# Kernel tuning notes

Measured on AMD Instinct MI355X. Metric: run time of the kernel, lower is better.

## Reference

```python
import jax, jax.numpy as jnp
import numpy as np

NQ, NS, QN, SN = 10000, 500, 4, 10   # num_question, num_skill, q/s neighbor sizes
B, S, D = 32, 200, 128               # batch, seq_len, emb_dim
HOPS = 3


def setup_inputs() -> dict:
    key = jax.random.key(0)
    ks = iter(jax.random.split(key, 40))

    def nrm(shape, scale=0.05):
        return jax.random.normal(next(ks), shape, dtype=jnp.float32) * scale

    return {
        "question": jax.random.randint(next(ks), (B, S), 0, NQ),
        "response": jax.random.randint(next(ks), (B, S), 0, 2),
        "mask": jnp.ones((B, S), dtype=jnp.int32),
        "q_neighbors": jax.random.randint(next(ks), (NQ, QN), 0, NS),  # question -> skill ids
        "s_neighbors": jax.random.randint(next(ks), (NS, SN), 0, NQ),  # skill -> question ids
        "qs_skills": jax.random.randint(next(ks), (NQ, 4), 0, NS),     # related skills per question
        "emb_q": nrm((NQ, D), 1.0),
        "emb_s": nrm((NS, D), 1.0),
        "emb_r": nrm((2, D), 1.0),
        "W_ih": nrm((2 * D, 4 * D)), "b_ih": nrm((4 * D,)), "b_hh": nrm((4 * D,)),
        "ft_W": nrm((D, D)), "ft_b": nrm((D,)),
        "agg_W": nrm((HOPS, D, D)), "agg_b": nrm((HOPS, D)),
        "last_W": nrm((D, D)), "last_b": nrm((D,)),
        "q_W": nrm((D, D)), "q_b": nrm((D,)),
        "k_W": nrm((D, D)), "k_b": nrm((D,)),
        "w_W": nrm((2 * D,)), "w_b": nrm(()),
    }


def reference(question, response, mask, q_neighbors, s_neighbors, qs_skills,
              emb_q, emb_s, emb_r, W_ih, b_ih, b_hh, ft_W, ft_b,
              agg_W, agg_b, last_W, last_b, q_W, q_b, k_W, k_b, w_W, w_b):
    # ---- multi-hop GNN aggregation for every (b, t) question (mask == 1 everywhere) ----
    q_flat = question.reshape(-1)              # [B*S]
    lvl1 = q_neighbors[q_flat]                 # [N, QN]            skill ids
    lvl2 = s_neighbors[lvl1]                   # [N, QN, SN]        question ids
    lvl3 = q_neighbors[lvl2]                   # [N, QN, SN, QN]    skill ids
    embs = [emb_q[q_flat], emb_s[lvl1], emb_q[lvl2], emb_s[lvl3]]
    for i in range(HOPS):
        embs = [jnp.tanh((embs[j] + embs[j + 1].mean(axis=-2)) @ agg_W[j] + agg_b[j])
                for j in range(HOPS - i)]
    agg_emb = jnp.tanh(embs[0] @ last_W + last_b).reshape(B, S, D)

    # ---- per-step input + zero-state LSTMCell (source calls lstm_cell without hx) ----
    q_trans = jax.nn.relu(agg_emb @ ft_W + ft_b)
    x = jnp.concatenate([q_trans, emb_r[response]], axis=-1)   # [B, S, 2D]
    gates = x @ W_ih + b_ih + b_hh                             # h_prev = 0, c_prev = 0
    i_g, f_g, g_g, o_g = jnp.split(gates, 4, axis=-1)
    c = jax.nn.sigmoid(i_g) * jnp.tanh(g_g)
    h = jax.nn.sigmoid(o_g) * jnp.tanh(c)                      # [B, S, D]
    states = h[:, :S - 1]                                      # state written at step t

    # ---- soft-recap attention prediction for q_next = question[:, t+1] ----
    q_next = question[:, 1:]                                   # [B, T], T = S-1
    qs = jnp.concatenate([emb_q[q_next][:, :, None, :], emb_s[qs_skills[q_next]]], axis=2)  # [B,T,5,D]

    inner = jnp.einsum('bnd,btmd->btnm', states, qs)           # state/qs inner products
    a_state = (states @ q_W + q_b) @ w_W[:D]                   # [B, N]  MLP_query on states
    a_qs = (qs @ k_W + k_b) @ w_W[D:]                          # [B, T, 5] MLP_key on qs
    logits = a_state[:, None, :, None] + a_qs[:, :, None, :] + w_b  # [B, T, N, 5]

    t_idx = jnp.arange(S - 1)
    valid = t_idx[None, :] <= t_idx[:, None]                   # [T, N]: states 0..t visible at t
    logits = jnp.where(valid[None, :, :, None], logits, -jnp.inf)
    alpha = jax.nn.softmax(logits.reshape(B, S - 1, -1), axis=-1).reshape(logits.shape)
    pred = jnp.sum(alpha * jax.nn.sigmoid(inner), axis=(2, 3))  # [B, T]

    return jnp.zeros((B, S), jnp.float32).at[:, 1:].set(pred)
```

## Files before the change

### kernel.cpp

```cpp
#include <hip/hip_runtime.h>

typedef unsigned short u16;
typedef unsigned int   u32;

#define NQd 10000
#define NSd 500
#define Bd  32
#define Sd  200
#define Td  199
#define Dd  128
#define NR  6368
#define PB  208

typedef __attribute__((ext_vector_type(8))) short bf16x8;
typedef __attribute__((ext_vector_type(4))) float f32x4;

__device__ __forceinline__ float sigf(float x) {
  return __builtin_amdgcn_rcpf(1.f + __expf(-x));
}
__device__ __forceinline__ float tanh_f(float x) {
  float ax = fminf(fabsf(x), 15.f);
  float e = __expf(2.f * ax);
  float r = 1.f - 2.f * __builtin_amdgcn_rcpf(e + 1.f);
  return copysignf(r, x);
}
__device__ __forceinline__ float bf2f(u16 u) { return __uint_as_float(((u32)u) << 16); }
__device__ __forceinline__ u16 f2bf(float f) {
  u32 b = __float_as_uint(f);
  b += 0x7FFFu + ((b >> 16) & 1u);
  return (u16)(b >> 16);
}
__device__ __forceinline__ void unp2(u32 u, float &a, float &b) {
  a = __uint_as_float(u << 16);
  b = __uint_as_float(u & 0xffff0000u);
}
__device__ __forceinline__ void unpack16(uint4 a0, uint4 a1, float* f) {
  unp2(a0.x, f[0], f[1]);  unp2(a0.y, f[2], f[3]);
  unp2(a0.z, f[4], f[5]);  unp2(a0.w, f[6], f[7]);
  unp2(a1.x, f[8], f[9]);  unp2(a1.y, f[10], f[11]);
  unp2(a1.z, f[12], f[13]); unp2(a1.w, f[14], f[15]);
}

struct Args {
  const int *question, *response, *q_nb, *s_nb, *qs_sk;
  const float *emb_q, *emb_s, *emb_r;
  const float *W_ih, *b_ih, *b_hh, *ft_W, *ft_b, *agg_W, *agg_b, *last_W, *last_b;
  const float *q_W, *q_b, *k_W, *k_b, *w_W;
  u16 *tabA, *tabB, *tabC, *tabs1, *tabs2, *states, *embq_bf, *embs_bf, *wts, *wiht;
  float *a_state, *qw, *kw, *scal, *er_part, *ev, *invZ, *pred_acc, *pm;
  int *qid_map, *resp_map;
};

#define SMEM_U16 21760

__device__ __forceinline__ void mfma_accum(const u16* Al, const u16* Wl,
                                           int l15, int quad, int cw, f32x4 acc[2][2])
{
#pragma unroll
  for (int kc = 0; kc < 4; ++kc) {
    const int ko = kc * 32 + quad * 8;
    bf16x8 af[2], bfv[2];
    af[0]  = *(const bf16x8*)&Al[l15 * 136 + ko];
    af[1]  = *(const bf16x8*)&Al[(16 + l15) * 136 + ko];
    bfv[0] = *(const bf16x8*)&Wl[(cw + l15) * 136 + ko];
    bfv[1] = *(const bf16x8*)&Wl[(cw + 16 + l15) * 136 + ko];
#pragma unroll
    for (int mt = 0; mt < 2; ++mt)
#pragma unroll
      for (int nt = 0; nt < 2; ++nt)
        acc[mt][nt] = __builtin_amdgcn_mfma_f32_16x16x32_bf16(af[mt], bfv[nt], acc[mt][nt], 0, 0, 0);
  }
}

__device__ __forceinline__ void zero_acc(f32x4 acc[2][2]) {
#pragma unroll
  for (int x = 0; x < 2; ++x)
#pragma unroll
    for (int y = 0; y < 2; ++y) acc[x][y] = (f32x4){0.f, 0.f, 0.f, 0.f};
}

__device__ __forceinline__ void stage_A(const u16* Atab, const u16* Btab,
                                        const int* nbr, int K, int tile0, int rows,
                                        int tid, u16* Al)
{
  int r = tid & 31, k0 = (tid >> 5) * 16;
  int row = tile0 + r; if (row >= rows) row = rows - 1;
  const u16* ap = Atab + (long)row * 128 + k0;
  if (K == 0) {
    *(uint4*)&Al[r * 136 + k0]     = *(const uint4*)ap;
    *(uint4*)&Al[r * 136 + k0 + 8] = *(const uint4*)(ap + 8);
  } else {
    float f[16];
    unpack16(*(const uint4*)ap, *(const uint4*)(ap + 8), f);
    float s[16];
#pragma unroll
    for (int q = 0; q < 16; ++q) s[q] = 0.f;
    for (int l = 0; l < K; ++l) {
      int id = nbr[(long)row * K + l];
      const u16* np = Btab + (long)id * 128 + k0;
      float g[16];
      unpack16(*(const uint4*)np, *(const uint4*)(np + 8), g);
#pragma unroll
      for (int q = 0; q < 16; ++q) s[q] += g[q];
    }
    float inv = 1.f / (float)K;
#pragma unroll
    for (int q = 0; q < 16; ++q) f[q] += s[q] * inv;
    u32 p[8];
#pragma unroll
    for (int q = 0; q < 8; ++q)
      p[q] = (u32)f2bf(f[2 * q]) | ((u32)f2bf(f[2 * q + 1]) << 16);
    *(uint4*)&Al[r * 136 + k0]     = make_uint4(p[0], p[1], p[2], p[3]);
    *(uint4*)&Al[r * 136 + k0 + 8] = make_uint4(p[4], p[5], p[6], p[7]);
  }
}

__device__ __forceinline__ void stage_W(const u16* Wt, int tid, u16* Wl)
{
  for (int i = tid; i < 2048; i += 256) {
    int col = i >> 4, seg = i & 15;
    *(uint4*)&Wl[col * 136 + seg * 8] = *(const uint4*)&Wt[(long)col * 128 + seg * 8];
  }
}

__device__ __forceinline__ void epi_tanh_global(const f32x4 acc[2][2], const float* cbias,
                                                u16* out, int rows, int tile0,
                                                int l15, int quad, int cw)
{
#pragma unroll
  for (int nt = 0; nt < 2; ++nt) {
    int col = cw + nt * 16 + l15;
    float cb = cbias[col];
#pragma unroll
    for (int mt = 0; mt < 2; ++mt) {
      int rbase = tile0 + mt * 16 + quad * 4;
#pragma unroll
      for (int i = 0; i < 4; ++i) {
        int row = rbase + i;
        if (row >= rows) continue;
        out[(long)row * 128 + col] = f2bf(tanh_f(acc[mt][nt][i] + cb));
      }
    }
  }
}

__device__ __forceinline__ void gemm_tile(
    const u16* __restrict__ Atab, const u16* __restrict__ Btab,
    const int* __restrict__ nbr, int K,
    const u16* __restrict__ Wt, const float* __restrict__ cbias,
    u16* __restrict__ out, int rows, int tile0, int tid, u16* smem)
{
  u16* Wl = smem;
  u16* Al = smem + 17408;
  stage_W(Wt, tid, Wl);
  stage_A(Atab, Btab, nbr, K, tile0, rows, tid, Al);
  __syncthreads();
  const int lane = tid & 63, wv = tid >> 6;
  const int l15 = lane & 15, quad = lane >> 4, cw = wv * 32;
  f32x4 acc[2][2];
  zero_acc(acc);
  mfma_accum(Al, Wl, l15, quad, cw, acc);
  epi_tanh_global(acc, cbias, out, rows, tile0, l15, quad, cw);
}

__global__ __launch_bounds__(256) void prep_all(Args a)
{
  const int T = gridDim.x * 256;
  for (int i = blockIdx.x * 256 + threadIdx.x; i < 491106; i += T) {
    if (i < 320000) {
      float4 v = *(const float4*)&a.emb_q[(long)i * 4];
      ((uint2*)a.embq_bf)[i] = make_uint2(
          (u32)f2bf(v.x) | ((u32)f2bf(v.y) << 16),
          (u32)f2bf(v.z) | ((u32)f2bf(v.w) << 16));
    } else if (i < 336000) {
      int c = i - 320000;
      float4 v = *(const float4*)&a.emb_s[(long)c * 4];
      ((uint2*)a.embs_bf)[c] = make_uint2(
          (u32)f2bf(v.x) | ((u32)f2bf(v.y) << 16),
          (u32)f2bf(v.z) | ((u32)f2bf(v.w) << 16));
    } else if (i < 417920) {
      int e = i - 336000;
      int seg = e >> 14, r = e & 16383;
      int col = r >> 7, k = r & 127;
      const float* src = (seg < 3) ? (a.agg_W + seg * 16384)
                                   : (seg == 3 ? a.last_W : a.ft_W);
      a.wts[e] = f2bf(src[k * 128 + col]);
    } else if (i < 483456) {
      int e = i - 417920;
      int col = e >> 7, k = e & 127;
      a.wiht[e] = f2bf(a.W_ih[k * 512 + col]);
    } else if (i < 489824) {
      int j = i - 483456;
      int b = j / Td, s = j - b * Td;
      a.qid_map[j]  = a.question[b * Sd + s];
      a.resp_map[j] = a.response[b * Sd + s];
    } else {
      int s = i - 489824;
      if (s < 128) {
        float acc = 0;
        for (int e = 0; e < 128; ++e) acc += a.q_W[s * 128 + e] * a.w_W[e];
        a.qw[s] = acc;
      } else if (s < 256) {
        int d = s - 128; float acc = 0;
        for (int e = 0; e < 128; ++e) acc += a.k_W[d * 128 + e] * a.w_W[128 + e];
        a.kw[d] = acc;
      } else if (s == 256) {
        float acc = 0;
        for (int e = 0; e < 128; ++e) acc += a.q_b[e] * a.w_W[e];
        a.scal[0] = acc;
      } else if (s == 257) {
        float acc = 0;
        for (int e = 0; e < 128; ++e) acc += a.k_b[e] * a.w_W[128 + e];
        a.scal[1] = acc;
      } else {
        int e2 = s - 258, rr = e2 >> 9, col = e2 & 511;
        float acc = a.b_ih[col] + a.b_hh[col];
        for (int d = 0; d < 128; ++d) acc += a.emb_r[rr * Dd + d] * a.W_ih[(128 + d) * 512 + col];
        a.er_part[rr * 512 + col] = acc;
      }
    }
  }
}

__global__ __launch_bounds__(256) void level1m(Args a)
{
  __shared__ __align__(16) u16 smem[SMEM_U16];
  const int i = blockIdx.x, tid = threadIdx.x;
  if (i >= 313) {
    gemm_tile(a.embs_bf, a.embq_bf, a.s_nb, 10, a.wts + 16384,
              a.agg_b + 128, a.tabs1, NSd, (i - 313) * 32, tid, smem);
    return;
  }
  u16* Wl = smem;
  u16* Al = smem + 17408;
  const int tile0 = i * 32;
  const int lane = tid & 63, wv = tid >> 6;
  const int l15 = lane & 15, quad = lane >> 4, cw = wv * 32;
  f32x4 acc[2][2];
  stage_W(a.wts + 2 * 16384, tid, Wl);
  stage_A(a.embq_bf, a.embs_bf, a.q_nb, 4, tile0, NQd, tid, Al);
  __syncthreads();
  zero_acc(acc);
  mfma_accum(Al, Wl, l15, quad, cw, acc);
  epi_tanh_global(acc, a.agg_b + 256, a.tabA, NQd, tile0, l15, quad, cw);
  __syncthreads();
  stage_W(a.wts, tid, Wl);
  __syncthreads();
  zero_acc(acc);
  mfma_accum(Al, Wl, l15, quad, cw, acc);
  epi_tanh_global(acc, a.agg_b, a.tabB, NQd, tile0, l15, quad, cw);
}

__global__ __launch_bounds__(256) void level2(Args a)
{
  __shared__ __align__(16) u16 smem[SMEM_U16];
  const int i = blockIdx.x, tid = threadIdx.x;
  if (i < 16)
    gemm_tile(a.tabs1, a.tabA, a.s_nb, 10, a.wts + 16384,
              a.agg_b + 128, a.tabs2, NSd, i * 32, tid, smem);
  else
    gemm_tile(a.tabB, a.tabs1, a.q_nb, 4, a.wts,
              a.agg_b, a.tabC, NQd, (i - 16) * 32, tid, smem);
}

__global__ __launch_bounds__(256) void chain3(Args a)
{
  __shared__ __align__(16) u16 smem[SMEM_U16];
  u16* Wl = smem;
  u16* Al = smem + 17408;
  const int tid = threadIdx.x;
  const int tile0 = blockIdx.x * 32;
  const int lane = tid & 63, wv = tid >> 6;
  const int l15 = lane & 15, quad = lane >> 4, cw = wv * 32;
  f32x4 acc[2][2];

  stage_W(a.wts, tid, Wl);
  stage_A(a.tabC, a.tabs2, a.q_nb, 4, tile0, NQd, tid, Al);
  __syncthreads();
  zero_acc(acc);
  mfma_accum(Al, Wl, l15, quad, cw, acc);
  __syncthreads();
#pragma unroll
  for (int nt = 0; nt < 2; ++nt) {
    int col = cw + nt * 16 + l15;
    float cb = a.agg_b[col];
#pragma unroll
    for (int mt = 0; mt < 2; ++mt)
#pragma unroll
      for (int i = 0; i < 4; ++i) {
        int rL = mt * 16 + quad * 4 + i;
        Al[rL * 136 + col] = f2bf(tanh_f(acc[mt][nt][i] + cb));
      }
  }
  stage_W(a.wts + 3 * 16384, tid, Wl);
  __syncthreads();

  zero_acc(acc);
  mfma_accum(Al, Wl, l15, quad, cw, acc);
  __syncthreads();
#pragma unroll
  for (int nt = 0; nt < 2; ++nt) {
    int col = cw + nt * 16 + l15;
    float cb = a.last_b[col];
#pragma unroll
    for (int mt = 0; mt < 2; ++mt)
#pragma unroll
      for (int i = 0; i < 4; ++i) {
        int rL = mt * 16 + quad * 4 + i;
        Al[rL * 136 + col] = f2bf(tanh_f(acc[mt][nt][i] + cb));
      }
  }
  stage_W(a.wts + 4 * 16384, tid, Wl);
  __syncthreads();

  zero_acc(acc);
  mfma_accum(Al, Wl, l15, quad, cw, acc);
#pragma unroll
  for (int nt = 0; nt < 2; ++nt) {
    int col = cw + nt * 16 + l15;
    float cb = a.ft_b[col];
#pragma unroll
    for (int mt = 0; mt < 2; ++mt) {
      int rbase = tile0 + mt * 16 + quad * 4;
#pragma unroll
      for (int i = 0; i < 4; ++i) {
        int row = rbase + i;
        if (row >= NQd) continue;
        a.tabA[(long)row * 128 + col] = f2bf(fmaxf(acc[mt][nt][i] + cb, 0.f));
      }
    }
  }
}

__global__ __launch_bounds__(256) void gates_k(Args a)
{
  __shared__ __align__(16) u16 smem[SMEM_U16];
  u16* Wl = smem;
  u16* Al = smem + 17408;
  const int tid = threadIdx.x;
  const int tile0 = blockIdx.x * 32;
  {
    int r = tid & 31, k0 = (tid >> 5) * 16;
    int row = tile0 + r;
    int arow = a.qid_map[row];
    const u16* ap = a.tabA + (long)arow * 128 + k0;
    *(uint4*)&Al[r * 136 + k0]     = *(const uint4*)ap;
    *(uint4*)&Al[r * 136 + k0 + 8] = *(const uint4*)(ap + 8);
  }
  const int lane = tid & 63, wv = tid >> 6;
  const int l15 = lane & 15, quad = lane >> 4, cw = wv * 32;
  f32x4 acc[3][2][2];
  const int goff[3] = {0, 256, 384};
#pragma unroll
  for (int p = 0; p < 3; ++p) {
    __syncthreads();
    stage_W(a.wiht + (long)goff[p] * 128, tid, Wl);
    __syncthreads();
    zero_acc(acc[p]);
    mfma_accum(Al, Wl, l15, quad, cw, acc[p]);
  }
  __syncthreads();
  float* hb = (float*)Wl;
#pragma unroll
  for (int nt = 0; nt < 2; ++nt) {
    int colL = cw + nt * 16 + l15;
#pragma unroll
    for (int mt = 0; mt < 2; ++mt) {
#pragma unroll
      for (int i = 0; i < 4; ++i) {
        int rL = mt * 16 + quad * 4 + i;
        int row = tile0 + rL;
        const float* rb = a.er_part + (long)a.resp_map[row] * 512;
        float iv = acc[0][mt][nt][i] + rb[colL];
        float gv = acc[1][mt][nt][i] + rb[256 + colL];
        float ov = acc[2][mt][nt][i] + rb[384 + colL];
        float c = sigf(iv) * tanh_f(gv);
        float h = sigf(ov) * tanh_f(c);
        a.states[(long)row * 128 + colL] = f2bf(h);
        hb[rL * 132 + colL] = h;
      }
    }
  }
  __syncthreads();
#pragma unroll
  for (int rr = 0; rr < 8; ++rr) {
    int rL = wv * 8 + rr;
    float p = hb[rL * 132 + lane] * a.qw[lane] + hb[rL * 132 + 64 + lane] * a.qw[64 + lane];
#pragma unroll
    for (int off = 32; off > 0; off >>= 1) p += __shfl_xor(p, off);
    if (lane == 0) a.a_state[tile0 + rL] = p + a.scal[0];
  }
}

__global__ __launch_bounds__(256) void bprep(Args a)
{
  __shared__ float red[256];
  __shared__ float evl[256];
  __shared__ float kwl[128];
  const int b = blockIdx.x, tid = threadIdx.x;
  if (tid < 128) kwl[tid] = a.kw[tid];
  float v = (tid < Td) ? a.a_state[b * Td + tid] : -1e30f;
  red[tid] = v; __syncthreads();
  for (int s = 128; s > 0; s >>= 1) { if (tid < s) red[tid] = fmaxf(red[tid], red[tid + s]); __syncthreads(); }
  float gmax = red[0];
  float e = (tid < Td) ? __expf(v - gmax) : 0.f;
  evl[tid] = e;
  if (tid < Td) { a.ev[b * PB + tid] = e; a.pred_acc[b * PB + tid] = 0.f; }
  __syncthreads();
  if (tid < Td) {
    float Z = 0.f;
    for (int n = 0; n <= tid; ++n) Z += evl[n];
    a.invZ[b * PB + tid] = 1.f / Z;
    int qn = a.question[b * Sd + tid + 1];
    float am[5];
#pragma unroll
    for (int m = 0; m < 5; ++m) {
      const u16* src = (m == 0) ? a.embq_bf + (long)qn * 128
                                : a.embs_bf + (long)a.qs_sk[qn * 4 + (m - 1)] * 128;
      float s = 0.f;
      for (int k = 0; k < 128; k += 8) {
        uint4 u = *(const uint4*)&src[k];
        float f[8];
        unp2(u.x, f[0], f[1]); unp2(u.y, f[2], f[3]);
        unp2(u.z, f[4], f[5]); unp2(u.w, f[6], f[7]);
#pragma unroll
        for (int q = 0; q < 8; ++q) s = fmaf(f[q], kwl[k + q], s);
      }
      am[m] = s + a.scal[1];
    }
    float mx = am[0];
#pragma unroll
    for (int m = 1; m < 5; ++m) mx = fmaxf(mx, am[m]);
    float ex[5], z = 0.f;
#pragma unroll
    for (int m = 0; m < 5; ++m) { ex[m] = __expf(am[m] - mx); z += ex[m]; }
    float iz = 1.f / z;
#pragma unroll
    for (int m = 0; m < 5; ++m) a.pm[((long)b * PB + tid) * 5 + m] = ex[m] * iz;
  }
}

__global__ __launch_bounds__(256) void gk_pred(Args a)
{
  const int n0 = blockIdx.x * 32;
  const int c0 = blockIdx.y * 128;
  const int b  = blockIdx.z;
  int c_hi = c0 + 127; if (c_hi > 994) c_hi = 994;
  const int tmax = c_hi / 5, tmin = c0 / 5;
  if (n0 > tmax) return;

  __shared__ __align__(16) u16 smem[SMEM_U16];
  __shared__ float predl[32];
  u16* Ql = smem;
  u16* Sl = smem + 17408;
  const int tid = threadIdx.x;
  if (tid < 32) predl[tid] = 0.f;
  {
    int r = tid & 31, k0 = (tid >> 5) * 16;
    int n = n0 + r; if (n > 198) n = 198;
    const u16* sp = a.states + ((long)b * Td + n) * 128 + k0;
    *(uint4*)&Sl[r * 136 + k0]     = *(const uint4*)sp;
    *(uint4*)&Sl[r * 136 + k0 + 8] = *(const uint4*)(sp + 8);
  }
  {
    int j = tid >> 1, k0 = (tid & 1) * 64;
    int col = c0 + j;
    uint4* dst = (uint4*)&Ql[j * 136 + k0];
    if (col < 995) {
      int t = col / 5, m = col - t * 5;
      int qn = a.question[b * Sd + t + 1];
      const u16* src = (m == 0) ? a.embq_bf + (long)qn * 128
                                : a.embs_bf + (long)a.qs_sk[qn * 4 + (m - 1)] * 128;
      src += k0;
#pragma unroll
      for (int q = 0; q < 8; ++q) dst[q] = ((const uint4*)src)[q];
    } else {
      uint4 z = make_uint4(0, 0, 0, 0);
#pragma unroll
      for (int q = 0; q < 8; ++q) dst[q] = z;
    }
  }
  __syncthreads();
  const int lane = tid & 63, wv = tid >> 6;
  const int l15 = lane & 15, quad = lane >> 4, cw = wv * 32;
  f32x4 acc[2][2];
  zero_acc(acc);
  mfma_accum(Sl, Ql, l15, quad, cw, acc);

#pragma unroll
  for (int nt = 0; nt < 2; ++nt) {
    int col = c0 + cw + nt * 16 + l15;
    if (col >= 995) continue;
    int t = col / 5, m = col - t * 5;
    float pmv = a.pm[((long)b * PB + t) * 5 + m];
    float part = 0.f;
#pragma unroll
    for (int mt = 0; mt < 2; ++mt) {
      int nb = n0 + mt * 16 + quad * 4;
      if (nb > t) continue;
      float4 ev4 = *(const float4*)&a.ev[b * PB + nb];
      float evv[4] = {ev4.x, ev4.y, ev4.z, ev4.w};
#pragma unroll
      for (int i = 0; i < 4; ++i) {
        int n = nb + i;
        if (n > t || n > 198) continue;
        part += evv[i] * sigf(acc[mt][nt][i]);
      }
    }
    part *= pmv;
    if (part != 0.f) atomicAdd(&predl[t - tmin], part);
  }
  __syncthreads();
  const int tcnt = tmax - tmin + 1;
  if (tid < tcnt) {
    float pv = predl[tid];
    if (pv != 0.f) atomicAdd(&a.pred_acc[b * PB + tmin + tid], pv);
  }
}

__global__ __launch_bounds__(256) void finalize(Args a, float* __restrict__ out)
{
  int i = blockIdx.x * 256 + threadIdx.x;
  if (i >= Bd * Sd) return;
  int b = i / Sd, s = i - b * Sd;
  out[i] = (s == 0) ? 0.f : a.pred_acc[b * PB + s - 1] * a.invZ[b * PB + s - 1];
}

extern "C" void kernel_launch(void* const* d_in, const int* in_sizes, int n_in,
                              void* d_out, int out_size, void* d_ws, size_t ws_size,
                              hipStream_t stream)
{
  Args a;
  a.question = (const int*)d_in[0];
  a.response = (const int*)d_in[1];
  a.q_nb     = (const int*)d_in[3];
  a.s_nb     = (const int*)d_in[4];
  a.qs_sk    = (const int*)d_in[5];
  a.emb_q    = (const float*)d_in[6];
  a.emb_s    = (const float*)d_in[7];
  a.emb_r    = (const float*)d_in[8];
  a.W_ih     = (const float*)d_in[9];
  a.b_ih     = (const float*)d_in[10];
  a.b_hh     = (const float*)d_in[11];
  a.ft_W     = (const float*)d_in[12];
  a.ft_b     = (const float*)d_in[13];
  a.agg_W    = (const float*)d_in[14];
  a.agg_b    = (const float*)d_in[15];
  a.last_W   = (const float*)d_in[16];
  a.last_b   = (const float*)d_in[17];
  a.q_W      = (const float*)d_in[18];
  a.q_b      = (const float*)d_in[19];
  a.k_W      = (const float*)d_in[20];
  a.k_b      = (const float*)d_in[21];
  a.w_W      = (const float*)d_in[22];

  u16* wsu = (u16*)d_ws;
  const long NT = 1280000, ST = 64000, RT = (long)NR * Dd;
  a.tabA  = wsu;
  a.tabB  = a.tabA + NT;
  a.tabC  = a.tabB + NT;
  a.tabs1 = a.tabC + NT;
  a.tabs2 = a.tabs1 + ST;
  a.states  = a.tabs2 + ST;
  a.embq_bf = a.states + RT;
  a.embs_bf = a.embq_bf + NT;
  a.wts     = a.embs_bf + ST;
  a.wiht    = a.wts + 5 * 16384;
  float* fp = (float*)(a.wiht + 65536);
  a.a_state = fp;
  a.qw      = fp + 6368;
  a.kw      = fp + 6496;
  a.scal    = fp + 6624;
  a.er_part = fp + 6640;
  a.ev       = fp + 7664;
  a.invZ     = a.ev + 32 * PB;
  a.pred_acc = a.invZ + 32 * PB;
  a.pm       = a.pred_acc + 32 * PB;
  a.qid_map  = (int*)(a.pm + 32 * PB * 5);
  a.resp_map = a.qid_map + NR;

  float* out = (float*)d_out;

  prep_all<<<640, 256, 0, stream>>>(a);
  level1m<<<329, 256, 0, stream>>>(a);
  level2<<<329, 256, 0, stream>>>(a);
  chain3<<<313, 256, 0, stream>>>(a);
  gates_k<<<199, 256, 0, stream>>>(a);
  bprep<<<Bd, 256, 0, stream>>>(a);
  gk_pred<<<dim3(7, 8, Bd), 256, 0, stream>>>(a);
  finalize<<<25, 256, 0, stream>>>(a, out);
}
```

Before: 196.7 us.

## Shrink GNN GEMM tiles to 16 rows and fuse level2 into chain kernel

The GEMM tiles in the GNN kernels shrink from 32x128 with 256 threads to 16x128 with 128 threads, doubling the block count so more compute units are busy. The tabC computation from level2 moves into the chain kernel, which keeps the intermediate in shared memory and reuses the staged neighbor ids. This removes one launch and a global round trip, leaving only a small skill-level kernel (g1k) separate. The serial prefix sum in bprep becomes a parallel Hillis-Steele scan. In exchange, each block now reloads the 128x128 weight tile for only 16 rows, which halves weight reuse per load.

After: 213.4 us. 8.5% more time.

```diff
diff --git a/kernel.cpp b/kernel.cpp
--- a/kernel.cpp
+++ b/kernel.cpp
@@ -51,39 +51,22 @@
   int *qid_map, *resp_map;
 };
 
-#define SMEM_U16 21760
-
-__device__ __forceinline__ void mfma_accum(const u16* Al, const u16* Wl,
-                                           int l15, int quad, int cw, f32x4 acc[2][2])
-{
-#pragma unroll
-  for (int kc = 0; kc < 4; ++kc) {
-    const int ko = kc * 32 + quad * 8;
-    bf16x8 af[2], bfv[2];
-    af[0]  = *(const bf16x8*)&Al[l15 * 136 + ko];
-    af[1]  = *(const bf16x8*)&Al[(16 + l15) * 136 + ko];
-    bfv[0] = *(const bf16x8*)&Wl[(cw + l15) * 136 + ko];
-    bfv[1] = *(const bf16x8*)&Wl[(cw + 16 + l15) * 136 + ko];
-#pragma unroll
-    for (int mt = 0; mt < 2; ++mt)
-#pragma unroll
-      for (int nt = 0; nt < 2; ++nt)
-        acc[mt][nt] = __builtin_amdgcn_mfma_f32_16x16x32_bf16(af[mt], bfv[nt], acc[mt][nt], 0, 0, 0);
-  }
-}
-
-__device__ __forceinline__ void zero_acc(f32x4 acc[2][2]) {
-#pragma unroll
-  for (int x = 0; x < 2; ++x)
-#pragma unroll
-    for (int y = 0; y < 2; ++y) acc[x][y] = (f32x4){0.f, 0.f, 0.f, 0.f};
-}
-
-__device__ __forceinline__ void stage_A(const u16* Atab, const u16* Btab,
-                                        const int* nbr, int K, int tile0, int rows,
-                                        int tid, u16* Al)
-{
-  int r = tid & 31, k0 = (tid >> 5) * 16;
+#define SM16_U16 (128 * 136 + 16 * 136)
+
+__device__ __forceinline__ void stageW128(const u16* Wt, int tid, u16* Wl)
+{
+  for (int i = tid; i < 2048; i += 128) {
+    int col = i >> 4, seg = i & 15;
+    *(uint4*)&Wl[col * 136 + seg * 8] = *(const uint4*)&Wt[(long)col * 128 + seg * 8];
+  }
+}
+
+template <int K>
+__device__ __forceinline__ void stageA16(const u16* Atab, const u16* Btab,
+                                         const int* nbr, int tile0, int rows,
+                                         int tid, u16* Al, int* ids)
+{
+  int r = tid & 15, k0 = (tid >> 4) * 16;
   int row = tile0 + r; if (row >= rows) row = rows - 1;
   const u16* ap = Atab + (long)row * 128 + k0;
   if (K == 0) {
@@ -95,15 +78,17 @@
     float s[16];
 #pragma unroll
     for (int q = 0; q < 16; ++q) s[q] = 0.f;
+#pragma unroll
+    for (int l = 0; l < K; ++l) ids[l] = nbr[(long)row * K + l];
+#pragma unroll
     for (int l = 0; l < K; ++l) {
-      int id = nbr[(long)row * K + l];
-      const u16* np = Btab + (long)id * 128 + k0;
+      const u16* np = Btab + (long)ids[l] * 128 + k0;
       float g[16];
       unpack16(*(const uint4*)np, *(const uint4*)(np + 8), g);
 #pragma unroll
       for (int q = 0; q < 16; ++q) s[q] += g[q];
     }
-    float inv = 1.f / (float)K;
+    const float inv = 1.f / (float)K;
 #pragma unroll
     for (int q = 0; q < 16; ++q) f[q] += s[q] * inv;
     u32 p[8];
@@ -115,52 +100,80 @@
   }
 }
 
-__device__ __forceinline__ void stage_W(const u16* Wt, int tid, u16* Wl)
-{
-  for (int i = tid; i < 2048; i += 256) {
-    int col = i >> 4, seg = i & 15;
-    *(uint4*)&Wl[col * 136 + seg * 8] = *(const uint4*)&Wt[(long)col * 128 + seg * 8];
-  }
-}
-
-__device__ __forceinline__ void epi_tanh_global(const f32x4 acc[2][2], const float* cbias,
-                                                u16* out, int rows, int tile0,
-                                                int l15, int quad, int cw)
-{
-#pragma unroll
-  for (int nt = 0; nt < 2; ++nt) {
-    int col = cw + nt * 16 + l15;
-    float cb = cbias[col];
-#pragma unroll
-    for (int mt = 0; mt < 2; ++mt) {
-      int rbase = tile0 + mt * 16 + quad * 4;
-#pragma unroll
-      for (int i = 0; i < 4; ++i) {
-        int row = rbase + i;
-        if (row >= rows) continue;
-        out[(long)row * 128 + col] = f2bf(tanh_f(acc[mt][nt][i] + cb));
-      }
-    }
-  }
-}
-
-__device__ __forceinline__ void gemm_tile(
-    const u16* __restrict__ Atab, const u16* __restrict__ Btab,
-    const int* __restrict__ nbr, int K,
-    const u16* __restrict__ Wt, const float* __restrict__ cbias,
-    u16* __restrict__ out, int rows, int tile0, int tid, u16* smem)
-{
-  u16* Wl = smem;
-  u16* Al = smem + 17408;
-  stage_W(Wt, tid, Wl);
-  stage_A(Atab, Btab, nbr, K, tile0, rows, tid, Al);
-  __syncthreads();
-  const int lane = tid & 63, wv = tid >> 6;
-  const int l15 = lane & 15, quad = lane >> 4, cw = wv * 32;
-  f32x4 acc[2][2];
-  zero_acc(acc);
-  mfma_accum(Al, Wl, l15, quad, cw, acc);
-  epi_tanh_global(acc, cbias, out, rows, tile0, l15, quad, cw);
+__device__ __forceinline__ void updateA16(const u16* Btab, const int* ids, int tid, u16* Al)
+{
+  int r = tid & 15, k0 = (tid >> 4) * 16;
+  float f[16];
+  unpack16(*(const uint4*)&Al[r * 136 + k0], *(const uint4*)&Al[r * 136 + k0 + 8], f);
+  float s[16];
+#pragma unroll
+  for (int q = 0; q < 16; ++q) s[q] = 0.f;
+#pragma unroll
+  for (int l = 0; l < 4; ++l) {
+    const u16* np = Btab + (long)ids[l] * 128 + k0;
+    float g[16];
+    unpack16(*(const uint4*)np, *(const uint4*)(np + 8), g);
+#pragma unroll
+    for (int q = 0; q < 16; ++q) s[q] += g[q];
+  }
+#pragma unroll
+  for (int q = 0; q < 16; ++q) f[q] += s[q] * 0.25f;
+  u32 p[8];
+#pragma unroll
+  for (int q = 0; q < 8; ++q)
+    p[q] = (u32)f2bf(f[2 * q]) | ((u32)f2bf(f[2 * q + 1]) << 16);
+  *(uint4*)&Al[r * 136 + k0]     = make_uint4(p[0], p[1], p[2], p[3]);
+  *(uint4*)&Al[r * 136 + k0 + 8] = make_uint4(p[4], p[5], p[6], p[7]);
+}
+
+__device__ __forceinline__ void zero4(f32x4 acc[4]) {
+#pragma unroll
+  for (int nt = 0; nt < 4; ++nt) acc[nt] = (f32x4){0.f, 0.f, 0.f, 0.f};
+}
+
+__device__ __forceinline__ void mfma16(const u16* Al, const u16* Wl,
+                                       int l15, int quad, int cw4, f32x4 acc[4])
+{
+#pragma unroll
+  for (int kc = 0; kc < 4; ++kc) {
+    const int ko = kc * 32 + quad * 8;
+    bf16x8 af = *(const bf16x8*)&Al[l15 * 136 + ko];
+#pragma unroll
+    for (int nt = 0; nt < 4; ++nt)
+      acc[nt] = __builtin_amdgcn_mfma_f32_16x16x32_bf16(
+          af, *(const bf16x8*)&Wl[(cw4 + nt * 16 + l15) * 136 + ko], acc[nt], 0, 0, 0);
+  }
+}
+
+__device__ __forceinline__ void epi_tanh_G16(const f32x4 acc[4], const float* cb,
+                                             u16* out, int rows, int tile0,
+                                             int l15, int quad, int cw4)
+{
+#pragma unroll
+  for (int nt = 0; nt < 4; ++nt) {
+    int col = cw4 + nt * 16 + l15;
+    float c = cb[col];
+#pragma unroll
+    for (int i = 0; i < 4; ++i) {
+      int row = tile0 + quad * 4 + i;
+      if (row < rows) out[(long)row * 128 + col] = f2bf(tanh_f(acc[nt][i] + c));
+    }
+  }
+}
+
+__device__ __forceinline__ void epi_tanh_L16(const f32x4 acc[4], const float* cb,
+                                             u16* Al, int l15, int quad, int cw4)
+{
+#pragma unroll
+  for (int nt = 0; nt < 4; ++nt) {
+    int col = cw4 + nt * 16 + l15;
+    float c = cb[col];
+#pragma unroll
+    for (int i = 0; i < 4; ++i) {
+      int rL = quad * 4 + i;
+      Al[rL * 136 + col] = f2bf(tanh_f(acc[nt][i] + c));
+    }
+  }
 }
 
 __global__ __launch_bounds__(256) void prep_all(Args a)
@@ -222,125 +235,117 @@
   }
 }
 
-__global__ __launch_bounds__(256) void level1m(Args a)
-{
-  __shared__ __align__(16) u16 smem[SMEM_U16];
+__global__ __launch_bounds__(128) void level1m(Args a)
+{
+  __shared__ __align__(16) u16 smem[SM16_U16];
+  u16* Wl = smem;
+  u16* Al = smem + 128 * 136;
   const int i = blockIdx.x, tid = threadIdx.x;
-  if (i >= 313) {
-    gemm_tile(a.embs_bf, a.embq_bf, a.s_nb, 10, a.wts + 16384,
-              a.agg_b + 128, a.tabs1, NSd, (i - 313) * 32, tid, smem);
+  const int lane = tid & 63, wv = tid >> 6;
+  const int l15 = lane & 15, quad = lane >> 4, cw4 = wv * 64;
+  f32x4 acc[4];
+  int ids[10];
+  if (i >= 625) {
+    const int tile0 = (i - 625) * 16;
+    stageW128(a.wts + 16384, tid, Wl);
+    stageA16<10>(a.embs_bf, a.embq_bf, a.s_nb, tile0, NSd, tid, Al, ids);
+    __syncthreads();
+    zero4(acc);
+    mfma16(Al, Wl, l15, quad, cw4, acc);
+    epi_tanh_G16(acc, a.agg_b + 128, a.tabs1, NSd, tile0, l15, quad, cw4);
     return;
   }
+  const int tile0 = i * 16;
+  stageW128(a.wts + 2 * 16384, tid, Wl);
+  stageA16<4>(a.embq_bf, a.embs_bf, a.q_nb, tile0, NQd, tid, Al, ids);
+  __syncthreads();
+  zero4(acc);
+  mfma16(Al, Wl, l15, quad, cw4, acc);
+  epi_tanh_G16(acc, a.agg_b + 256, a.tabA, NQd, tile0, l15, quad, cw4);
+  __syncthreads();
+  stageW128(a.wts, tid, Wl);
+  __syncthreads();
+  zero4(acc);
+  mfma16(Al, Wl, l15, quad, cw4, acc);
+  epi_tanh_G16(acc, a.agg_b, a.tabB, NQd, tile0, l15, quad, cw4);
+}
+
+__global__ __launch_bounds__(128) void g1k(Args a)
+{
+  __shared__ __align__(16) u16 smem[SM16_U16];
   u16* Wl = smem;
-  u16* Al = smem + 17408;
-  const int tile0 = i * 32;
+  u16* Al = smem + 128 * 136;
+  const int tid = threadIdx.x;
+  const int tile0 = blockIdx.x * 16;
   const int lane = tid & 63, wv = tid >> 6;
-  const int l15 = lane & 15, quad = lane >> 4, cw = wv * 32;
-  f32x4 acc[2][2];
-  stage_W(a.wts + 2 * 16384, tid, Wl);
-  stage_A(a.embq_bf, a.embs_bf, a.q_nb, 4, tile0, NQd, tid, Al);
-  __syncthreads();
-  zero_acc(acc);
-  mfma_accum(Al, Wl, l15, quad, cw, acc);
-  epi_tanh_global(acc, a.agg_b + 256, a.tabA, NQd, tile0, l15, quad, cw);
-  __syncthreads();
-  stage_W(a.wts, tid, Wl);
-  __syncthreads();
-  zero_acc(acc);
-  mfma_accum(Al, Wl, l15, quad, cw, acc);
-  epi_tanh_global(acc, a.agg_b, a.tabB, NQd, tile0, l15, quad, cw);
-}
-
-__global__ __launch_bounds__(256) void level2(Args a)
-{
-  __shared__ __align__(16) u16 smem[SMEM_U16];
-  const int i = blockIdx.x, tid = threadIdx.x;
-  if (i < 16)
-    gemm_tile(a.tabs1, a.tabA, a.s_nb, 10, a.wts + 16384,
-              a.agg_b + 128, a.tabs2, NSd, i * 32, tid, smem);
-  else
-    gemm_tile(a.tabB, a.tabs1, a.q_nb, 4, a.wts,
-              a.agg_b, a.tabC, NQd, (i - 16) * 32, tid, smem);
-}
-
-__global__ __launch_bounds__(256) void chain3(Args a)
-{
-  __shared__ __align__(16) u16 smem[SMEM_U16];
+  const int l15 = lane & 15, quad = lane >> 4, cw4 = wv * 64;
+  f32x4 acc[4];
+  int ids[10];
+  stageW128(a.wts + 16384, tid, Wl);
+  stageA16<10>(a.tabs1, a.tabA, a.s_nb, tile0, NSd, tid, Al, ids);
+  __syncthreads();
+  zero4(acc);
+  mfma16(Al, Wl, l15, quad, cw4, acc);
+  epi_tanh_G16(acc, a.agg_b + 128, a.tabs2, NSd, tile0, l15, quad, cw4);
+}
+
+__global__ __launch_bounds__(128) void chain4(Args a)
+{
+  __shared__ __align__(16) u16 smem[SM16_U16];
   u16* Wl = smem;
-  u16* Al = smem + 17408;
+  u16* Al = smem + 128 * 136;
   const int tid = threadIdx.x;
-  const int tile0 = blockIdx.x * 32;
+  const int tile0 = blockIdx.x * 16;
   const int lane = tid & 63, wv = tid >> 6;
-  const int l15 = lane & 15, quad = lane >> 4, cw = wv * 32;
-  f32x4 acc[2][2];
-
-  stage_W(a.wts, tid, Wl);
-  stage_A(a.tabC, a.tabs2, a.q_nb, 4, tile0, NQd, tid, Al);
-  __syncthreads();
-  zero_acc(acc);
-  mfma_accum(Al, Wl, l15, quad, cw, acc);
-  __syncthreads();
-#pragma unroll
-  for (int nt = 0; nt < 2; ++nt) {
-    int col = cw + nt * 16 + l15;
-    float cb = a.agg_b[col];
-#pragma unroll
-    for (int mt = 0; mt < 2; ++mt)
-#pragma unroll
-      for (int i = 0; i < 4; ++i) {
-        int rL = mt * 16 + quad * 4 + i;
-        Al[rL * 136 + col] = f2bf(tanh_f(acc[mt][nt][i] + cb));
-      }
-  }
-  stage_W(a.wts + 3 * 16384, tid, Wl);
-  __syncthreads();
-
-  zero_acc(acc);
-  mfma_accum(Al, Wl, l15, quad, cw, acc);
-  __syncthreads();
-#pragma unroll
-  for (int nt = 0; nt < 2; ++nt) {
-    int col = cw + nt * 16 + l15;
-    float cb = a.last_b[col];
-#pragma unroll
-    for (int mt = 0; mt < 2; ++mt)
-#pragma unroll
-      for (int i = 0; i < 4; ++i) {
-        int rL = mt * 16 + quad * 4 + i;
-        Al[rL * 136 + col] = f2bf(tanh_f(acc[mt][nt][i] + cb));
-      }
-  }
-  stage_W(a.wts + 4 * 16384, tid, Wl);
-  __syncthreads();
-
-  zero_acc(acc);
-  mfma_accum(Al, Wl, l15, quad, cw, acc);
-#pragma unroll
-  for (int nt = 0; nt < 2; ++nt) {
-    int col = cw + nt * 16 + l15;
+  const int l15 = lane & 15, quad = lane >> 4, cw4 = wv * 64;
+  f32x4 acc[4];
+  int ids[4];
+
+  stageW128(a.wts, tid, Wl);
+  stageA16<4>(a.tabB, a.tabs1, a.q_nb, tile0, NQd, tid, Al, ids);
+  __syncthreads();
+  zero4(acc);
+  mfma16(Al, Wl, l15, quad, cw4, acc);
+  __syncthreads();
+  epi_tanh_L16(acc, a.agg_b, Al, l15, quad, cw4);
+  __syncthreads();
+  updateA16(a.tabs2, ids, tid, Al);
+  __syncthreads();
+  zero4(acc);
+  mfma16(Al, Wl, l15, quad, cw4, acc);
+  __syncthreads();
+  epi_tanh_L16(acc, a.agg_b, Al, l15, quad, cw4);
+  stageW128(a.wts + 3 * 16384, tid, Wl);
+  __syncthreads();
+  zero4(acc);
+  mfma16(Al, Wl, l15, quad, cw4, acc);
+  __syncthreads();
+  epi_tanh_L16(acc, a.last_b, Al, l15, quad, cw4);
+  stageW128(a.wts + 4 * 16384, tid, Wl);
+  __syncthreads();
+  zero4(acc);
+  mfma16(Al, Wl, l15, quad, cw4, acc);
+#pragma unroll
+  for (int nt = 0; nt < 4; ++nt) {
+    int col = cw4 + nt * 16 + l15;
     float cb = a.ft_b[col];
 #pragma unroll
-    for (int mt = 0; mt < 2; ++mt) {
-      int rbase = tile0 + mt * 16 + quad * 4;
-#pragma unroll
-      for (int i = 0; i < 4; ++i) {
-        int row = rbase + i;
-        if (row >= NQd) continue;
-        a.tabA[(long)row * 128 + col] = f2bf(fmaxf(acc[mt][nt][i] + cb, 0.f));
-      }
-    }
-  }
-}
-
-__global__ __launch_bounds__(256) void gates_k(Args a)
-{
-  __shared__ __align__(16) u16 smem[SMEM_U16];
+    for (int i = 0; i < 4; ++i) {
+      int row = tile0 + quad * 4 + i;
+      a.tabA[(long)row * 128 + col] = f2bf(fmaxf(acc[nt][i] + cb, 0.f));
+    }
+  }
+}
+
+__global__ __launch_bounds__(128) void gates_k(Args a)
+{
+  __shared__ __align__(16) u16 smem[SM16_U16];
   u16* Wl = smem;
-  u16* Al = smem + 17408;
+  u16* Al = smem + 128 * 136;
   const int tid = threadIdx.x;
-  const int tile0 = blockIdx.x * 32;
+  const int tile0 = blockIdx.x * 16;
   {
-    int r = tid & 31, k0 = (tid >> 5) * 16;
+    int r = tid & 15, k0 = (tid >> 4) * 16;
     int row = tile0 + r;
     int arow = a.qid_map[row];
     const u16* ap = a.tabA + (long)arow * 128 + k0;
@@ -348,37 +353,34 @@
     *(uint4*)&Al[r * 136 + k0 + 8] = *(const uint4*)(ap + 8);
   }
   const int lane = tid & 63, wv = tid >> 6;
-  const int l15 = lane & 15, quad = lane >> 4, cw = wv * 32;
-  f32x4 acc[3][2][2];
+  const int l15 = lane & 15, quad = lane >> 4, cw4 = wv * 64;
+  f32x4 acc[3][4];
   const int goff[3] = {0, 256, 384};
 #pragma unroll
   for (int p = 0; p < 3; ++p) {
     __syncthreads();
-    stage_W(a.wiht + (long)goff[p] * 128, tid, Wl);
+    stageW128(a.wiht + (long)goff[p] * 128, tid, Wl);
     __syncthreads();
-    zero_acc(acc[p]);
-    mfma_accum(Al, Wl, l15, quad, cw, acc[p]);
+    zero4(acc[p]);
+    mfma16(Al, Wl, l15, quad, cw4, acc[p]);
   }
   __syncthreads();
   float* hb = (float*)Wl;
 #pragma unroll
-  for (int nt = 0; nt < 2; ++nt) {
-    int colL = cw + nt * 16 + l15;
-#pragma unroll
-    for (int mt = 0; mt < 2; ++mt) {
-#pragma unroll
-      for (int i = 0; i < 4; ++i) {
-        int rL = mt * 16 + quad * 4 + i;
-        int row = tile0 + rL;
-        const float* rb = a.er_part + (long)a.resp_map[row] * 512;
-        float iv = acc[0][mt][nt][i] + rb[colL];
-        float gv = acc[1][mt][nt][i] + rb[256 + colL];
-        float ov = acc[2][mt][nt][i] + rb[384 + colL];
-        float c = sigf(iv) * tanh_f(gv);
-        float h = sigf(ov) * tanh_f(c);
-        a.states[(long)row * 128 + colL] = f2bf(h);
-        hb[rL * 132 + colL] = h;
-      }
+  for (int nt = 0; nt < 4; ++nt) {
+    int col = cw4 + nt * 16 + l15;
+#pragma unroll
+    for (int i = 0; i < 4; ++i) {
+      int rL = quad * 4 + i;
+      int row = tile0 + rL;
+      const float* rb = a.er_part + (long)a.resp_map[row] * 512;
+      float iv = acc[0][nt][i] + rb[col];
+      float gv = acc[1][nt][i] + rb[256 + col];
+      float ov = acc[2][nt][i] + rb[384 + col];
+      float c = sigf(iv) * tanh_f(gv);
+      float h = sigf(ov) * tanh_f(c);
+      a.states[(long)row * 128 + col] = f2bf(h);
+      hb[rL * 132 + col] = h;
     }
   }
   __syncthreads();
@@ -407,10 +409,14 @@
   evl[tid] = e;
   if (tid < Td) { a.ev[b * PB + tid] = e; a.pred_acc[b * PB + tid] = 0.f; }
   __syncthreads();
+  for (int off = 1; off < 256; off <<= 1) {
+    float add = (tid >= off) ? evl[tid - off] : 0.f;
+    __syncthreads();
+    evl[tid] += add;
+    __syncthreads();
+  }
   if (tid < Td) {
-    float Z = 0.f;
-    for (int n = 0; n <= tid; ++n) Z += evl[n];
-    a.invZ[b * PB + tid] = 1.f / Z;
+    a.invZ[b * PB + tid] = 1.f / evl[tid];
     int qn = a.question[b * Sd + tid + 1];
     float am[5];
 #pragma unroll
@@ -449,10 +455,10 @@
   const int tmax = c_hi / 5, tmin = c0 / 5;
   if (n0 > tmax) return;
 
-  __shared__ __align__(16) u16 smem[SMEM_U16];
+  __shared__ __align__(16) u16 smem[128 * 136 + 32 * 136];
   __shared__ float predl[32];
   u16* Ql = smem;
-  u16* Sl = smem + 17408;
+  u16* Sl = smem + 128 * 136;
   const int tid = threadIdx.x;
   if (tid < 32) predl[tid] = 0.f;
   {
@@ -482,10 +488,27 @@
   }
   __syncthreads();
   const int lane = tid & 63, wv = tid >> 6;
-  const int l15 = lane & 15, quad = lane >> 4, cw = wv * 32;
+  const int l15 = lane & 15, quad = lane >> 4;
+  const int cw = wv * 32;
   f32x4 acc[2][2];
-  zero_acc(acc);
-  mfma_accum(Sl, Ql, l15, quad, cw, acc);
+#pragma unroll
+  for (int x = 0; x < 2; ++x)
+#pragma unroll
+    for (int y = 0; y < 2; ++y) acc[x][y] = (f32x4){0.f, 0.f, 0.f, 0.f};
+#pragma unroll
+  for (int kc = 0; kc < 4; ++kc) {
+    const int ko = kc * 32 + quad * 8;
+    bf16x8 af[2], bfv[2];
+    af[0]  = *(const bf16x8*)&Sl[l15 * 136 + ko];
+    af[1]  = *(const bf16x8*)&Sl[(16 + l15) * 136 + ko];
+    bfv[0] = *(const bf16x8*)&Ql[(cw + l15) * 136 + ko];
+    bfv[1] = *(const bf16x8*)&Ql[(cw + 16 + l15) * 136 + ko];
+#pragma unroll
+    for (int mt = 0; mt < 2; ++mt)
+#pragma unroll
+      for (int nt = 0; nt < 2; ++nt)
+        acc[mt][nt] = __builtin_amdgcn_mfma_f32_16x16x32_bf16(af[mt], bfv[nt], acc[mt][nt], 0, 0, 0);
+  }
 
 #pragma unroll
   for (int nt = 0; nt < 2; ++nt) {
@@ -582,10 +605,10 @@
   float* out = (float*)d_out;
 
   prep_all<<<640, 256, 0, stream>>>(a);
-  level1m<<<329, 256, 0, stream>>>(a);
-  level2<<<329, 256, 0, stream>>>(a);
-  chain3<<<313, 256, 0, stream>>>(a);
-  gates_k<<<199, 256, 0, stream>>>(a);
+  level1m<<<657, 128, 0, stream>>>(a);
+  g1k<<<32, 128, 0, stream>>>(a);
+  chain4<<<625, 128, 0, stream>>>(a);
+  gates_k<<<398, 128, 0, stream>>>(a);
   bprep<<<Bd, 256, 0, stream>>>(a);
   gk_pred<<<dim3(7, 8, Bd), 256, 0, stream>>>(a);
   finalize<<<25, 256, 0, stream>>>(a, out);
```

## Fuse question-level hop-2 GEMM into chain kernel and scan softmax normaliser

Applied to the files above, without the earlier changes.

The level-2 GEMM over all questions, which wrote tabC to global memory, now runs inside the chain kernel. Its tanh output stays in LDS and the neighbour mean from tabs2 is added in place before the next hop, so the tabC round trip and its buffer go away. The level-2 launch shrinks to 16 skill-only blocks, and bprep replaces its O(T) per-thread prefix sum with a parallel Hillis-Steele scan in shared memory. In exchange, the chain kernel gains an extra GEMM and a dependent gather from tabs2, and the tiny g1k launch does little work and can leave the device mostly idle.

After: 197.5 us. About the same (+0.4%).

```diff
diff --git a/kernel.cpp b/kernel.cpp
--- a/kernel.cpp
+++ b/kernel.cpp
@@ -46,7 +46,7 @@
   const float *emb_q, *emb_s, *emb_r;
   const float *W_ih, *b_ih, *b_hh, *ft_W, *ft_b, *agg_W, *agg_b, *last_W, *last_b;
   const float *q_W, *q_b, *k_W, *k_b, *w_W;
-  u16 *tabA, *tabB, *tabC, *tabs1, *tabs2, *states, *embq_bf, *embs_bf, *wts, *wiht;
+  u16 *tabA, *tabB, *tabs1, *tabs2, *states, *embq_bf, *embs_bf, *wts, *wiht;
   float *a_state, *qw, *kw, *scal, *er_part, *ev, *invZ, *pred_acc, *pm;
   int *qid_map, *resp_map;
 };
@@ -115,6 +115,35 @@
   }
 }
 
+__device__ __forceinline__ void update_A(const u16* Btab, const int* nbr,
+                                         int tile0, int rows, int tid, u16* Al)
+{
+  int r = tid & 31, k0 = (tid >> 5) * 16;
+  int row = tile0 + r; if (row >= rows) row = rows - 1;
+  float f[16];
+  unpack16(*(const uint4*)&Al[r * 136 + k0], *(const uint4*)&Al[r * 136 + k0 + 8], f);
+  float s[16];
+#pragma unroll
+  for (int q = 0; q < 16; ++q) s[q] = 0.f;
+#pragma unroll
+  for (int l = 0; l < 4; ++l) {
+    int id = nbr[(long)row * 4 + l];
+    const u16* np = Btab + (long)id * 128 + k0;
+    float g[16];
+    unpack16(*(const uint4*)np, *(const uint4*)(np + 8), g);
+#pragma unroll
+    for (int q = 0; q < 16; ++q) s[q] += g[q];
+  }
+#pragma unroll
+  for (int q = 0; q < 16; ++q) f[q] += s[q] * 0.25f;
+  u32 p[8];
+#pragma unroll
+  for (int q = 0; q < 8; ++q)
+    p[q] = (u32)f2bf(f[2 * q]) | ((u32)f2bf(f[2 * q + 1]) << 16);
+  *(uint4*)&Al[r * 136 + k0]     = make_uint4(p[0], p[1], p[2], p[3]);
+  *(uint4*)&Al[r * 136 + k0 + 8] = make_uint4(p[4], p[5], p[6], p[7]);
+}
+
 __device__ __forceinline__ void stage_W(const u16* Wt, int tid, u16* Wl)
 {
   for (int i = tid; i < 2048; i += 256) {
@@ -141,6 +170,23 @@
         out[(long)row * 128 + col] = f2bf(tanh_f(acc[mt][nt][i] + cb));
       }
     }
+  }
+}
+
+__device__ __forceinline__ void epi_tanh_lds(const f32x4 acc[2][2], const float* cbias,
+                                             u16* Al, int l15, int quad, int cw)
+{
+#pragma unroll
+  for (int nt = 0; nt < 2; ++nt) {
+    int col = cw + nt * 16 + l15;
+    float cb = cbias[col];
+#pragma unroll
+    for (int mt = 0; mt < 2; ++mt)
+#pragma unroll
+      for (int i = 0; i < 4; ++i) {
+        int rL = mt * 16 + quad * 4 + i;
+        Al[rL * 136 + col] = f2bf(tanh_f(acc[mt][nt][i] + cb));
+      }
   }
 }
 
@@ -251,19 +297,15 @@
   epi_tanh_global(acc, a.agg_b, a.tabB, NQd, tile0, l15, quad, cw);
 }
 
-__global__ __launch_bounds__(256) void level2(Args a)
+__global__ __launch_bounds__(256) void g1k(Args a)
 {
   __shared__ __align__(16) u16 smem[SMEM_U16];
-  const int i = blockIdx.x, tid = threadIdx.x;
-  if (i < 16)
-    gemm_tile(a.tabs1, a.tabA, a.s_nb, 10, a.wts + 16384,
-              a.agg_b + 128, a.tabs2, NSd, i * 32, tid, smem);
-  else
-    gemm_tile(a.tabB, a.tabs1, a.q_nb, 4, a.wts,
-              a.agg_b, a.tabC, NQd, (i - 16) * 32, tid, smem);
-}
-
-__global__ __launch_bounds__(256) void chain3(Args a)
+  const int tid = threadIdx.x;
+  gemm_tile(a.tabs1, a.tabA, a.s_nb, 10, a.wts + 16384,
+            a.agg_b + 128, a.tabs2, NSd, blockIdx.x * 32, tid, smem);
+}
+
+__global__ __launch_bounds__(256) void chain4(Args a)
 {
   __shared__ __align__(16) u16 smem[SMEM_U16];
   u16* Wl = smem;
@@ -275,41 +317,27 @@
   f32x4 acc[2][2];
 
   stage_W(a.wts, tid, Wl);
-  stage_A(a.tabC, a.tabs2, a.q_nb, 4, tile0, NQd, tid, Al);
+  stage_A(a.tabB, a.tabs1, a.q_nb, 4, tile0, NQd, tid, Al);
   __syncthreads();
   zero_acc(acc);
   mfma_accum(Al, Wl, l15, quad, cw, acc);
   __syncthreads();
-#pragma unroll
-  for (int nt = 0; nt < 2; ++nt) {
-    int col = cw + nt * 16 + l15;
-    float cb = a.agg_b[col];
-#pragma unroll
-    for (int mt = 0; mt < 2; ++mt)
-#pragma unroll
-      for (int i = 0; i < 4; ++i) {
-        int rL = mt * 16 + quad * 4 + i;
-        Al[rL * 136 + col] = f2bf(tanh_f(acc[mt][nt][i] + cb));
-      }
-  }
+  epi_tanh_lds(acc, a.agg_b, Al, l15, quad, cw);
+  __syncthreads();
+
+  update_A(a.tabs2, a.q_nb, tile0, NQd, tid, Al);
+  __syncthreads();
+  zero_acc(acc);
+  mfma_accum(Al, Wl, l15, quad, cw, acc);
+  __syncthreads();
+  epi_tanh_lds(acc, a.agg_b, Al, l15, quad, cw);
   stage_W(a.wts + 3 * 16384, tid, Wl);
   __syncthreads();
 
   zero_acc(acc);
   mfma_accum(Al, Wl, l15, quad, cw, acc);
   __syncthreads();
-#pragma unroll
-  for (int nt = 0; nt < 2; ++nt) {
-    int col = cw + nt * 16 + l15;
-    float cb = a.last_b[col];
-#pragma unroll
-    for (int mt = 0; mt < 2; ++mt)
-#pragma unroll
-      for (int i = 0; i < 4; ++i) {
-        int rL = mt * 16 + quad * 4 + i;
-        Al[rL * 136 + col] = f2bf(tanh_f(acc[mt][nt][i] + cb));
-      }
-  }
+  epi_tanh_lds(acc, a.last_b, Al, l15, quad, cw);
   stage_W(a.wts + 4 * 16384, tid, Wl);
   __syncthreads();
 
@@ -407,10 +435,14 @@
   evl[tid] = e;
   if (tid < Td) { a.ev[b * PB + tid] = e; a.pred_acc[b * PB + tid] = 0.f; }
   __syncthreads();
+  for (int off = 1; off < 256; off <<= 1) {
+    float add = (tid >= off) ? evl[tid - off] : 0.f;
+    __syncthreads();
+    evl[tid] += add;
+    __syncthreads();
+  }
   if (tid < Td) {
-    float Z = 0.f;
-    for (int n = 0; n <= tid; ++n) Z += evl[n];
-    a.invZ[b * PB + tid] = 1.f / Z;
+    a.invZ[b * PB + tid] = 1.f / evl[tid];
     int qn = a.question[b * Sd + tid + 1];
     float am[5];
 #pragma unroll
@@ -558,8 +590,7 @@
   const long NT = 1280000, ST = 64000, RT = (long)NR * Dd;
   a.tabA  = wsu;
   a.tabB  = a.tabA + NT;
-  a.tabC  = a.tabB + NT;
-  a.tabs1 = a.tabC + NT;
+  a.tabs1 = a.tabB + NT;
   a.tabs2 = a.tabs1 + ST;
   a.states  = a.tabs2 + ST;
   a.embq_bf = a.states + RT;
@@ -583,8 +614,8 @@
 
   prep_all<<<640, 256, 0, stream>>>(a);
   level1m<<<329, 256, 0, stream>>>(a);
-  level2<<<329, 256, 0, stream>>>(a);
-  chain3<<<313, 256, 0, stream>>>(a);
+  g1k<<<16, 256, 0, stream>>>(a);
+  chain4<<<313, 256, 0, stream>>>(a);
   gates_k<<<199, 256, 0, stream>>>(a);
   bprep<<<Bd, 256, 0, stream>>>(a);
   gk_pred<<<dim3(7, 8, Bd), 256, 0, stream>>>(a);
```
